# Performance work log

Hardware: AMD Instinct MI355X
Metric: run time of the kernel (lower is better)

Reference implementation:

```python
import jax, jax.numpy as jnp
import numpy as np

S = 32  # spatial_size
EPS = 1e-8

def _adaptive_avg_pool(x, s):
    b, c, h, w = x.shape
    kh, kw = h // s, w // s
    return x.reshape(b, c, s, kh, s, kw).mean(axis=(3, 5))

def _gram_cosine(x):
    # x: [B, C, s, s] -> rows: [B*s*s, C]
    b, c, s, _ = x.shape
    rows = x.reshape(b, c, s * s).transpose(0, 2, 1).reshape(b * s * s, c)
    norms = jnp.sqrt(jnp.sum(rows * rows, axis=-1, keepdims=True))
    xn = rows / jnp.maximum(norms, EPS)
    return xn @ xn.T  # [N, N]

def setup_inputs() -> dict:
    key = jax.random.key(0)
    k1, k2 = jax.random.split(key)
    p1 = jax.random.normal(k1, (8, 64, 128, 128), dtype=jnp.float32)
    p2 = jax.random.normal(k2, (8, 64, 128, 128), dtype=jnp.float32)
    return {"p1": p1, "p2": p2}

def reference(p1, p2):
    sim_a = _gram_cosine(_adaptive_avg_pool(p1, S))
    sim_b = _gram_cosine(_adaptive_avg_pool(p2, S))
    return jnp.mean((sim_a - sim_b) ** 2)
```

## Files before the change

kernel.cpp:

```cpp
#include <hip/hip_runtime.h>

typedef float f4 __attribute__((ext_vector_type(4)));
typedef float f2 __attribute__((ext_vector_type(2)));

#define PAD 68
#define NPART 256
#define PART_STRIDE 12288


__global__ __launch_bounds__(1024) void fused_gram_kernel(
    const float* __restrict__ p1, const float* __restrict__ p2,
    float* __restrict__ partials, unsigned* __restrict__ cnt)
{
    __shared__ float la[32 * PAD];
    __shared__ float lb[32 * PAD];
    __shared__ float nred[64][17];
    __shared__ float sa[32], sb[32];
    const int t  = threadIdx.x;
    const int b  = blockIdx.x >> 5;
    const int oi = blockIdx.x & 31;

    if (blockIdx.x == 0 && t == 0) *cnt = 0u;

    #pragma unroll
    for (int k = 0; k < 2; ++k) {
        const int idx = k * 1024 + t;
        const int c   = idx >> 5;
        const int oj  = idx & 31;
        const long off = (long)((b * 64 + c) * 128 + oi * 4) * 128 + oj * 4;
        const float* s1 = p1 + off;
        const float* s2 = p2 + off;
        f4 va = *(const f4*)(s1) + *(const f4*)(s1 + 128)
              + *(const f4*)(s1 + 256) + *(const f4*)(s1 + 384);
        f4 vb = *(const f4*)(s2) + *(const f4*)(s2 + 128)
              + *(const f4*)(s2 + 256) + *(const f4*)(s2 + 384);
        la[oj * PAD + c] = ((va[0] + va[1]) + (va[2] + va[3])) * 0.0625f;
        lb[oj * PAD + c] = ((vb[0] + vb[1]) + (vb[2] + vb[3])) * 0.0625f;
    }
    __syncthreads();

    {
        const int r = t & 31, g = t >> 5;
        const int m = g >> 4, q = g & 15;
        const float* src = m ? lb : la;
        float ss = 0.f;
        #pragma unroll
        for (int j = 0; j < 4; ++j) {
            const float v = src[r * PAD + q * 4 + j];
            ss = fmaf(v, v, ss);
        }
        nred[m * 32 + r][q] = ss;
    }
    __syncthreads();
    if (t < 64) {
        const int m = t >> 5, r = t & 31;
        float ss = 0.f;
        #pragma unroll
        for (int q = 0; q < 16; ++q) ss += nred[m * 32 + r][q];
        const float rs = 1.0f / fmaxf(sqrtf(ss), 1e-8f);
        if (m) sb[r] = rs; else sa[r] = rs;
    }
    __syncthreads();

    #pragma unroll
    for (int k = 0; k < 2; ++k) {
        const int idx = k * 1024 + t;
        const int c = idx >> 5, oj = idx & 31;
        la[oj * PAD + c] *= sa[oj];
        lb[oj * PAD + c] *= sb[oj];
    }
    __syncthreads();

    const int c1 = (t >> 5) * 2;
    const int c2 = (t & 31) * 2;
    f2 aa0 = {}, aa1 = {}, ab0 = {}, ab1 = {}, bb0 = {}, bb1 = {};

    #pragma unroll 8
    for (int r = 0; r < 32; ++r) {
        const f2 a1 = *(const f2*)&la[r * PAD + c1];
        const f2 a2 = *(const f2*)&la[r * PAD + c2];
        const f2 b1 = *(const f2*)&lb[r * PAD + c1];
        const f2 b2 = *(const f2*)&lb[r * PAD + c2];
        aa0 += a2 * a1[0];  aa1 += a2 * a1[1];
        ab0 += b2 * a1[0];  ab1 += b2 * a1[1];
        bb0 += b2 * b1[0];  bb1 += b2 * b1[1];
    }

    float* P = partials + (long)blockIdx.x * PART_STRIDE;
    *(f2*)&P[0 * 4096 + (c1    ) * 64 + c2] = aa0;
    *(f2*)&P[0 * 4096 + (c1 + 1) * 64 + c2] = aa1;
    *(f2*)&P[1 * 4096 + (c1    ) * 64 + c2] = ab0;
    *(f2*)&P[1 * 4096 + (c1 + 1) * 64 + c2] = ab1;
    *(f2*)&P[2 * 4096 + (c1    ) * 64 + c2] = bb0;
    *(f2*)&P[2 * 4096 + (c1 + 1) * 64 + c2] = bb1;
}

__global__ __launch_bounds__(256) void reduce_kernel(
    const float* __restrict__ partials, float* __restrict__ bpart,
    unsigned* __restrict__ cnt, float* __restrict__ out)
{
    __shared__ float red[3][16][17];
    __shared__ float vred[16];
    __shared__ float fr[256];
    __shared__ unsigned last_flag;
    const int t  = threadIdx.x;
    const int el = t & 15;
    const int pc = t >> 4;
    const int e  = blockIdx.x * 16 + el;

    float saa = 0.f, sab = 0.f, sbb = 0.f;
    #pragma unroll 4
    for (int i = 0; i < 16; ++i) {
        const float* P = partials + (long)(pc * 16 + i) * PART_STRIDE;
        saa += P[e];
        sab += P[4096 + e];
        sbb += P[8192 + e];
    }
    red[0][el][pc] = saa; red[1][el][pc] = sab; red[2][el][pc] = sbb;
    __syncthreads();

    if (t < 16) {
        float a = 0.f, m = 0.f, bv = 0.f;
        #pragma unroll
        for (int p = 0; p < 16; ++p) {
            a  += red[0][t][p];
            m  += red[1][t][p];
            bv += red[2][t][p];
        }
        vred[t] = fmaf(a, a, fmaf(bv, bv, -2.0f * (m * m)));
    }
    __syncthreads();

    if (t == 0) {
        float s = 0.f;
        #pragma unroll
        for (int i = 0; i < 16; ++i) s += vred[i];
        __hip_atomic_store(&bpart[blockIdx.x], s, __ATOMIC_RELEASE,
                           __HIP_MEMORY_SCOPE_AGENT);
        unsigned old = __hip_atomic_fetch_add(cnt, 1u, __ATOMIC_ACQ_REL,
                                              __HIP_MEMORY_SCOPE_AGENT);
        last_flag = (old == NPART - 1) ? 1u : 0u;
    }
    __syncthreads();

    if (last_flag) {
        fr[t] = __hip_atomic_load(&bpart[t], __ATOMIC_ACQUIRE,
                                  __HIP_MEMORY_SCOPE_AGENT);
        __syncthreads();
        for (int s2 = 128; s2 > 0; s2 >>= 1) {
            if (t < s2) fr[t] += fr[t + s2];
            __syncthreads();
        }
        if (t == 0) out[0] = fr[0] * (1.0f / 67108864.0f);
    }
}

extern "C" void kernel_launch(void* const* d_in, const int* in_sizes, int n_in,
                              void* d_out, int out_size, void* d_ws, size_t ws_size,
                              hipStream_t stream)
{
    const float* p1 = (const float*)d_in[0];
    const float* p2 = (const float*)d_in[1];
    float* ws       = (float*)d_ws;
    float* partials = ws;
    float* bpart    = ws + (long)NPART * PART_STRIDE;
    unsigned* cnt   = (unsigned*)(bpart + NPART);

    fused_gram_kernel<<<NPART, 1024, 0, stream>>>(p1, p2, partials, cnt);
    reduce_kernel   <<<NPART, 256, 0, stream>>>(partials, bpart, cnt, (float*)d_out);
}
```

Before: 35.19 us.

## Fuse gram and reduction kernels with a grid-wide spin barrier and transposed partials

Merges the two kernels into one, using an atomic counter spin barrier so that all 256 blocks finish writing partials before the cross-block reduction starts. Partials are stored transposed (element-major, block-minor) so that each wavefront can read 256 contiguous values and reduce them with shuffles. The counter is reset with a memset node instead of inside the kernel. This removes one kernel launch and the shared-memory staging of the reduction. In exchange the scattered stride-256 stores become uncoalesced, and the spin barrier relies on all 256 blocks of 1024 threads being co-resident.

```diff
diff --git a/kernel.cpp b/kernel.cpp
--- a/kernel.cpp
+++ b/kernel.cpp
@@ -4,23 +4,25 @@
 typedef float f2 __attribute__((ext_vector_type(2)));
 
 #define PAD 68
-#define NPART 256
-#define PART_STRIDE 12288
+#define NBLK 256
 
 
-__global__ __launch_bounds__(1024) void fused_gram_kernel(
+__global__ __launch_bounds__(1024) void fused_all_kernel(
     const float* __restrict__ p1, const float* __restrict__ p2,
-    float* __restrict__ partials, unsigned* __restrict__ cnt)
+    float* __restrict__ pT, float* __restrict__ bpart,
+    unsigned* __restrict__ cnt, float* __restrict__ out)
 {
     __shared__ float la[32 * PAD];
     __shared__ float lb[32 * PAD];
     __shared__ float nred[64][17];
     __shared__ float sa[32], sb[32];
-    const int t  = threadIdx.x;
-    const int b  = blockIdx.x >> 5;
-    const int oi = blockIdx.x & 31;
-
-    if (blockIdx.x == 0 && t == 0) *cnt = 0u;
+    __shared__ float vred[16];
+    __shared__ float fr[256];
+    __shared__ unsigned lastf;
+    const int t   = threadIdx.x;
+    const int blk = blockIdx.x;
+    const int b   = blk >> 5;
+    const int oi  = blk & 31;
 
     #pragma unroll
     for (int k = 0; k < 2; ++k) {
@@ -86,48 +88,52 @@
         bb0 += b2 * b1[0];  bb1 += b2 * b1[1];
     }
 
-    float* P = partials + (long)blockIdx.x * PART_STRIDE;
-    *(f2*)&P[0 * 4096 + (c1    ) * 64 + c2] = aa0;
-    *(f2*)&P[0 * 4096 + (c1 + 1) * 64 + c2] = aa1;
-    *(f2*)&P[1 * 4096 + (c1    ) * 64 + c2] = ab0;
-    *(f2*)&P[1 * 4096 + (c1 + 1) * 64 + c2] = ab1;
-    *(f2*)&P[2 * 4096 + (c1    ) * 64 + c2] = bb0;
-    *(f2*)&P[2 * 4096 + (c1 + 1) * 64 + c2] = bb1;
-}
+    {
+        const int e0 = c1 * 64 + c2;
+        const int e1 = e0 + 64;
+        pT[(0 * 4096 + e0    ) * 256 + blk] = aa0[0];
+        pT[(0 * 4096 + e0 + 1) * 256 + blk] = aa0[1];
+        pT[(0 * 4096 + e1    ) * 256 + blk] = aa1[0];
+        pT[(0 * 4096 + e1 + 1) * 256 + blk] = aa1[1];
+        pT[(1 * 4096 + e0    ) * 256 + blk] = ab0[0];
+        pT[(1 * 4096 + e0 + 1) * 256 + blk] = ab0[1];
+        pT[(1 * 4096 + e1    ) * 256 + blk] = ab1[0];
+        pT[(1 * 4096 + e1 + 1) * 256 + blk] = ab1[1];
+        pT[(2 * 4096 + e0    ) * 256 + blk] = bb0[0];
+        pT[(2 * 4096 + e0 + 1) * 256 + blk] = bb0[1];
+        pT[(2 * 4096 + e1    ) * 256 + blk] = bb1[0];
+        pT[(2 * 4096 + e1 + 1) * 256 + blk] = bb1[1];
+    }
 
-__global__ __launch_bounds__(256) void reduce_kernel(
-    const float* __restrict__ partials, float* __restrict__ bpart,
-    unsigned* __restrict__ cnt, float* __restrict__ out)
-{
-    __shared__ float red[3][16][17];
-    __shared__ float vred[16];
-    __shared__ float fr[256];
-    __shared__ unsigned last_flag;
-    const int t  = threadIdx.x;
-    const int el = t & 15;
-    const int pc = t >> 4;
-    const int e  = blockIdx.x * 16 + el;
-
-    float saa = 0.f, sab = 0.f, sbb = 0.f;
-    #pragma unroll 4
-    for (int i = 0; i < 16; ++i) {
-        const float* P = partials + (long)(pc * 16 + i) * PART_STRIDE;
-        saa += P[e];
-        sab += P[4096 + e];
-        sbb += P[8192 + e];
+    __syncthreads();
+    if (t == 0) {
+        __hip_atomic_fetch_add(cnt, 1u, __ATOMIC_ACQ_REL,
+                               __HIP_MEMORY_SCOPE_AGENT);
+        while (__hip_atomic_load(cnt, __ATOMIC_ACQUIRE,
+                                 __HIP_MEMORY_SCOPE_AGENT) < NBLK) {}
     }
-    red[0][el][pc] = saa; red[1][el][pc] = sab; red[2][el][pc] = sbb;
     __syncthreads();
 
-    if (t < 16) {
-        float a = 0.f, m = 0.f, bv = 0.f;
+    {
+        const int w = t >> 6;
+        const int l = t & 63;
+        const int e = blk * 16 + w;
+        float s3[3];
         #pragma unroll
-        for (int p = 0; p < 16; ++p) {
-            a  += red[0][t][p];
-            m  += red[1][t][p];
-            bv += red[2][t][p];
+        for (int g = 0; g < 3; ++g) {
+            const f4 v = *(const f4*)&pT[((g * 4096 + e) * 256) + l * 4];
+            float s = (v[0] + v[1]) + (v[2] + v[3]);
+            s += __shfl_xor(s, 1);
+            s += __shfl_xor(s, 2);
+            s += __shfl_xor(s, 4);
+            s += __shfl_xor(s, 8);
+            s += __shfl_xor(s, 16);
+            s += __shfl_xor(s, 32);
+            s3[g] = s;
         }
-        vred[t] = fmaf(a, a, fmaf(bv, bv, -2.0f * (m * m)));
+        if (l == 0)
+            vred[w] = fmaf(s3[0], s3[0],
+                      fmaf(s3[2], s3[2], -2.0f * (s3[1] * s3[1])));
     }
     __syncthreads();
 
@@ -135,17 +141,18 @@
         float s = 0.f;
         #pragma unroll
         for (int i = 0; i < 16; ++i) s += vred[i];
-        __hip_atomic_store(&bpart[blockIdx.x], s, __ATOMIC_RELEASE,
+        __hip_atomic_store(&bpart[blk], s, __ATOMIC_RELEASE,
                            __HIP_MEMORY_SCOPE_AGENT);
-        unsigned old = __hip_atomic_fetch_add(cnt, 1u, __ATOMIC_ACQ_REL,
+        unsigned old = __hip_atomic_fetch_add(cnt + 1, 1u, __ATOMIC_ACQ_REL,
                                               __HIP_MEMORY_SCOPE_AGENT);
-        last_flag = (old == NPART - 1) ? 1u : 0u;
+        lastf = (old == NBLK - 1) ? 1u : 0u;
     }
     __syncthreads();
 
-    if (last_flag) {
-        fr[t] = __hip_atomic_load(&bpart[t], __ATOMIC_ACQUIRE,
-                                  __HIP_MEMORY_SCOPE_AGENT);
+    if (lastf) {
+        if (t < 256)
+            fr[t] = __hip_atomic_load(&bpart[t], __ATOMIC_ACQUIRE,
+                                      __HIP_MEMORY_SCOPE_AGENT);
         __syncthreads();
         for (int s2 = 128; s2 > 0; s2 >>= 1) {
             if (t < s2) fr[t] += fr[t + s2];
@@ -161,11 +168,12 @@
 {
     const float* p1 = (const float*)d_in[0];
     const float* p2 = (const float*)d_in[1];
-    float* ws       = (float*)d_ws;
-    float* partials = ws;
-    float* bpart    = ws + (long)NPART * PART_STRIDE;
-    unsigned* cnt   = (unsigned*)(bpart + NPART);
+    float* ws    = (float*)d_ws;
+    float* pT    = ws;
+    float* bpart = ws + 3 * 4096 * 256;
+    unsigned* cnt = (unsigned*)(bpart + 256);
 
-    fused_gram_kernel<<<NPART, 1024, 0, stream>>>(p1, p2, partials, cnt);
-    reduce_kernel   <<<NPART, 256, 0, stream>>>(partials, bpart, cnt, (float*)d_out);
+    hipMemsetAsync(cnt, 0, 2 * sizeof(unsigned), stream);
+    fused_all_kernel<<<NBLK, 1024, 0, stream>>>(p1, p2, pT, bpart, cnt,
+                                                (float*)d_out);
 }
```

New measurement: 107.1 us. 3.04x slower.

## Split each pooled row across two blocks to double grid parallelism

Applied to the files above, without the earlier changes.

The gram kernel now launches 512 blocks of 512 threads, each handling half of a pooled row (16 spatial positions) instead of a full row, with f4-wide register tiles in the 64x64 channel-gram accumulation. This fills more CUs on the MI355X and uses wider LDS loads and global stores. In exchange the partial-sum buffer doubles, so the reduction kernel reads twice as many partials (32 per thread) and there is more global write and read traffic.

```diff
diff --git a/kernel.cpp b/kernel.cpp
--- a/kernel.cpp
+++ b/kernel.cpp
@@ -4,43 +4,46 @@
 typedef float f2 __attribute__((ext_vector_type(2)));
 
 #define PAD 68
-#define NPART 256
+#define NPART 512
 #define PART_STRIDE 12288
+#define NBLK2 256
 
 
-__global__ __launch_bounds__(1024) void fused_gram_kernel(
+__global__ __launch_bounds__(512) void fused_gram_kernel(
     const float* __restrict__ p1, const float* __restrict__ p2,
     float* __restrict__ partials, unsigned* __restrict__ cnt)
 {
-    __shared__ float la[32 * PAD];
-    __shared__ float lb[32 * PAD];
-    __shared__ float nred[64][17];
-    __shared__ float sa[32], sb[32];
-    const int t  = threadIdx.x;
-    const int b  = blockIdx.x >> 5;
-    const int oi = blockIdx.x & 31;
+    __shared__ float la[16 * PAD];
+    __shared__ float lb[16 * PAD];
+    __shared__ float nred[32][17];
+    __shared__ float sa[16], sb[16];
+    const int t   = threadIdx.x;
+    const int blk = blockIdx.x;
+    const int b   = blk >> 6;
+    const int oi  = (blk & 63) >> 1;
+    const int h   = blk & 1;
 
-    if (blockIdx.x == 0 && t == 0) *cnt = 0u;
+    if (blk == 0 && t == 0) *cnt = 0u;
 
     #pragma unroll
-    for (int k = 0; k < 2; ++k) {
-        const int idx = k * 1024 + t;
-        const int c   = idx >> 5;
-        const int oj  = idx & 31;
-        const long off = (long)((b * 64 + c) * 128 + oi * 4) * 128 + oj * 4;
-        const float* s1 = p1 + off;
-        const float* s2 = p2 + off;
-        f4 va = *(const f4*)(s1) + *(const f4*)(s1 + 128)
-              + *(const f4*)(s1 + 256) + *(const f4*)(s1 + 384);
-        f4 vb = *(const f4*)(s2) + *(const f4*)(s2 + 128)
-              + *(const f4*)(s2 + 256) + *(const f4*)(s2 + 384);
-        la[oj * PAD + c] = ((va[0] + va[1]) + (va[2] + va[3])) * 0.0625f;
-        lb[oj * PAD + c] = ((vb[0] + vb[1]) + (vb[2] + vb[3])) * 0.0625f;
+    for (int k = 0; k < 4; ++k) {
+        const int idx  = k * 512 + t;
+        const int m    = idx >> 10;
+        const int rest = idx & 1023;
+        const int c    = rest >> 4;
+        const int oj16 = rest & 15;
+        const long off = (long)((b * 64 + c) * 128 + oi * 4) * 128
+                       + (h * 16 + oj16) * 4;
+        const float* s = (m ? p2 : p1) + off;
+        f4 v = *(const f4*)(s) + *(const f4*)(s + 128)
+             + *(const f4*)(s + 256) + *(const f4*)(s + 384);
+        float* dst = m ? lb : la;
+        dst[oj16 * PAD + c] = ((v[0] + v[1]) + (v[2] + v[3])) * 0.0625f;
     }
     __syncthreads();
 
     {
-        const int r = t & 31, g = t >> 5;
+        const int r = t & 15, g = t >> 4;
         const int m = g >> 4, q = g & 15;
         const float* src = m ? lb : la;
         float ss = 0.f;
@@ -49,50 +52,53 @@
             const float v = src[r * PAD + q * 4 + j];
             ss = fmaf(v, v, ss);
         }
-        nred[m * 32 + r][q] = ss;
+        nred[m * 16 + r][q] = ss;
     }
     __syncthreads();
-    if (t < 64) {
-        const int m = t >> 5, r = t & 31;
+    if (t < 32) {
+        const int m = t >> 4, r = t & 15;
         float ss = 0.f;
         #pragma unroll
-        for (int q = 0; q < 16; ++q) ss += nred[m * 32 + r][q];
+        for (int q = 0; q < 16; ++q) ss += nred[m * 16 + r][q];
         const float rs = 1.0f / fmaxf(sqrtf(ss), 1e-8f);
         if (m) sb[r] = rs; else sa[r] = rs;
     }
     __syncthreads();
 
     #pragma unroll
-    for (int k = 0; k < 2; ++k) {
-        const int idx = k * 1024 + t;
-        const int c = idx >> 5, oj = idx & 31;
-        la[oj * PAD + c] *= sa[oj];
-        lb[oj * PAD + c] *= sb[oj];
+    for (int k = 0; k < 4; ++k) {
+        const int idx  = k * 512 + t;
+        const int m    = idx >> 10;
+        const int rest = idx & 1023;
+        const int r    = rest >> 6;
+        const int c    = rest & 63;
+        if (m) lb[r * PAD + c] *= sb[r];
+        else   la[r * PAD + c] *= sa[r];
     }
     __syncthreads();
 
-    const int c1 = (t >> 5) * 2;
-    const int c2 = (t & 31) * 2;
-    f2 aa0 = {}, aa1 = {}, ab0 = {}, ab1 = {}, bb0 = {}, bb1 = {};
+    const int c1 = (t >> 4) * 2;
+    const int c2 = (t & 15) * 4;
+    f4 aa0 = {}, aa1 = {}, ab0 = {}, ab1 = {}, bb0 = {}, bb1 = {};
 
     #pragma unroll 8
-    for (int r = 0; r < 32; ++r) {
+    for (int r = 0; r < 16; ++r) {
         const f2 a1 = *(const f2*)&la[r * PAD + c1];
-        const f2 a2 = *(const f2*)&la[r * PAD + c2];
+        const f4 a2 = *(const f4*)&la[r * PAD + c2];
         const f2 b1 = *(const f2*)&lb[r * PAD + c1];
-        const f2 b2 = *(const f2*)&lb[r * PAD + c2];
+        const f4 b2 = *(const f4*)&lb[r * PAD + c2];
         aa0 += a2 * a1[0];  aa1 += a2 * a1[1];
         ab0 += b2 * a1[0];  ab1 += b2 * a1[1];
         bb0 += b2 * b1[0];  bb1 += b2 * b1[1];
     }
 
-    float* P = partials + (long)blockIdx.x * PART_STRIDE;
-    *(f2*)&P[0 * 4096 + (c1    ) * 64 + c2] = aa0;
-    *(f2*)&P[0 * 4096 + (c1 + 1) * 64 + c2] = aa1;
-    *(f2*)&P[1 * 4096 + (c1    ) * 64 + c2] = ab0;
-    *(f2*)&P[1 * 4096 + (c1 + 1) * 64 + c2] = ab1;
-    *(f2*)&P[2 * 4096 + (c1    ) * 64 + c2] = bb0;
-    *(f2*)&P[2 * 4096 + (c1 + 1) * 64 + c2] = bb1;
+    float* P = partials + (long)blk * PART_STRIDE;
+    *(f4*)&P[0 * 4096 + (c1    ) * 64 + c2] = aa0;
+    *(f4*)&P[0 * 4096 + (c1 + 1) * 64 + c2] = aa1;
+    *(f4*)&P[1 * 4096 + (c1    ) * 64 + c2] = ab0;
+    *(f4*)&P[1 * 4096 + (c1 + 1) * 64 + c2] = ab1;
+    *(f4*)&P[2 * 4096 + (c1    ) * 64 + c2] = bb0;
+    *(f4*)&P[2 * 4096 + (c1 + 1) * 64 + c2] = bb1;
 }
 
 __global__ __launch_bounds__(256) void reduce_kernel(
@@ -110,8 +116,8 @@
 
     float saa = 0.f, sab = 0.f, sbb = 0.f;
     #pragma unroll 4
-    for (int i = 0; i < 16; ++i) {
-        const float* P = partials + (long)(pc * 16 + i) * PART_STRIDE;
+    for (int i = 0; i < 32; ++i) {
+        const float* P = partials + (long)(pc * 32 + i) * PART_STRIDE;
         saa += P[e];
         sab += P[4096 + e];
         sbb += P[8192 + e];
@@ -139,7 +145,7 @@
                            __HIP_MEMORY_SCOPE_AGENT);
         unsigned old = __hip_atomic_fetch_add(cnt, 1u, __ATOMIC_ACQ_REL,
                                               __HIP_MEMORY_SCOPE_AGENT);
-        last_flag = (old == NPART - 1) ? 1u : 0u;
+        last_flag = (old == NBLK2 - 1) ? 1u : 0u;
     }
     __syncthreads();
 
@@ -164,8 +170,8 @@
     float* ws       = (float*)d_ws;
     float* partials = ws;
     float* bpart    = ws + (long)NPART * PART_STRIDE;
-    unsigned* cnt   = (unsigned*)(bpart + NPART);
+    unsigned* cnt   = (unsigned*)(bpart + NBLK2);
 
-    fused_gram_kernel<<<NPART, 1024, 0, stream>>>(p1, p2, partials, cnt);
-    reduce_kernel   <<<NPART, 256, 0, stream>>>(partials, bpart, cnt, (float*)d_out);
+    fused_gram_kernel<<<NPART, 512, 0, stream>>>(p1, p2, partials, cnt);
+    reduce_kernel   <<<NBLK2, 256, 0, stream>>>(partials, bpart, cnt, (float*)d_out);
 }
```

Measured after the change: 37.64 us. 7.0% more time.

## Pipeline pooling loads with gram accumulation in four column chunks using double-buffered LDS

Applied to the files above, without the earlier changes.

Splits each block's 32 pooled columns into four chunks of 8 and double-buffers them in shared memory, issuing global loads for the next chunk before running the gram accumulation on the current one. Row normalization now uses a wave-wide shuffle reduction instead of a two-stage shared-memory reduction, and barriers use a raw waitcnt+s_barrier helper. The intent is to hide HBM load latency behind FMA work and cut synchronization overhead, at the cost of more barriers and register pressure for in-flight loads.

```diff
diff --git a/kernel.cpp b/kernel.cpp
--- a/kernel.cpp
+++ b/kernel.cpp
@@ -8,83 +8,98 @@
 #define PART_STRIDE 12288
 
 
+__device__ __forceinline__ void lds_barrier() {
+    asm volatile("s_waitcnt lgkmcnt(0)" ::: "memory");
+    __builtin_amdgcn_s_barrier();
+    __builtin_amdgcn_sched_barrier(0);
+}
+
 __global__ __launch_bounds__(1024) void fused_gram_kernel(
     const float* __restrict__ p1, const float* __restrict__ p2,
     float* __restrict__ partials, unsigned* __restrict__ cnt)
 {
-    __shared__ float la[32 * PAD];
-    __shared__ float lb[32 * PAD];
-    __shared__ float nred[64][17];
-    __shared__ float sa[32], sb[32];
+    __shared__ float la[2][8 * PAD];
+    __shared__ float lb[2][8 * PAD];
     const int t  = threadIdx.x;
     const int b  = blockIdx.x >> 5;
     const int oi = blockIdx.x & 31;
 
     if (blockIdx.x == 0 && t == 0) *cnt = 0u;
 
-    #pragma unroll
-    for (int k = 0; k < 2; ++k) {
-        const int idx = k * 1024 + t;
-        const int c   = idx >> 5;
-        const int oj  = idx & 31;
-        const long off = (long)((b * 64 + c) * 128 + oi * 4) * 128 + oj * 4;
-        const float* s1 = p1 + off;
-        const float* s2 = p2 + off;
-        f4 va = *(const f4*)(s1) + *(const f4*)(s1 + 128)
-              + *(const f4*)(s1 + 256) + *(const f4*)(s1 + 384);
-        f4 vb = *(const f4*)(s2) + *(const f4*)(s2 + 128)
-              + *(const f4*)(s2 + 256) + *(const f4*)(s2 + 384);
-        la[oj * PAD + c] = ((va[0] + va[1]) + (va[2] + va[3])) * 0.0625f;
-        lb[oj * PAD + c] = ((vb[0] + vb[1]) + (vb[2] + vb[3])) * 0.0625f;
-    }
-    __syncthreads();
+    const int m   = t >> 9;
+    const int c   = (t >> 3) & 63;
+    const int oj8 = t & 7;
+    const float* src = m ? p2 : p1;
+    const long base = (long)((b * 64 + c) * 128 + oi * 4) * 128 + oj8 * 4;
+    float* dst0 = m ? lb[0] : la[0];
+    float* dst1 = m ? lb[1] : la[1];
 
-    {
-        const int r = t & 31, g = t >> 5;
-        const int m = g >> 4, q = g & 15;
-        const float* src = m ? lb : la;
-        float ss = 0.f;
-        #pragma unroll
-        for (int j = 0; j < 4; ++j) {
-            const float v = src[r * PAD + q * 4 + j];
-            ss = fmaf(v, v, ss);
-        }
-        nred[m * 32 + r][q] = ss;
-    }
-    __syncthreads();
-    if (t < 64) {
-        const int m = t >> 5, r = t & 31;
-        float ss = 0.f;
-        #pragma unroll
-        for (int q = 0; q < 16; ++q) ss += nred[m * 32 + r][q];
-        const float rs = 1.0f / fmaxf(sqrtf(ss), 1e-8f);
-        if (m) sb[r] = rs; else sa[r] = rs;
-    }
-    __syncthreads();
-
-    #pragma unroll
-    for (int k = 0; k < 2; ++k) {
-        const int idx = k * 1024 + t;
-        const int c = idx >> 5, oj = idx & 31;
-        la[oj * PAD + c] *= sa[oj];
-        lb[oj * PAD + c] *= sb[oj];
-    }
-    __syncthreads();
+    const int l  = t & 63;
+    const int w  = t >> 6;
+    const int nm = w >> 3, nr = w & 7;
 
     const int c1 = (t >> 5) * 2;
     const int c2 = (t & 31) * 2;
     f2 aa0 = {}, aa1 = {}, ab0 = {}, ab1 = {}, bb0 = {}, bb1 = {};
 
-    #pragma unroll 8
-    for (int r = 0; r < 32; ++r) {
-        const f2 a1 = *(const f2*)&la[r * PAD + c1];
-        const f2 a2 = *(const f2*)&la[r * PAD + c2];
-        const f2 b1 = *(const f2*)&lb[r * PAD + c1];
-        const f2 b2 = *(const f2*)&lb[r * PAD + c2];
-        aa0 += a2 * a1[0];  aa1 += a2 * a1[1];
-        ab0 += b2 * a1[0];  ab1 += b2 * a1[1];
-        bb0 += b2 * b1[0];  bb1 += b2 * b1[1];
-    }
+    auto issue = [&](int q, f4& R0, f4& R1, f4& R2, f4& R3) {
+        const float* s = src + base + q * 32;
+        R0 = *(const f4*)(s);
+        R1 = *(const f4*)(s + 128);
+        R2 = *(const f4*)(s + 256);
+        R3 = *(const f4*)(s + 384);
+    };
+    auto pool = [&](const f4& R0, const f4& R1, const f4& R2, const f4& R3,
+                    float* dst) {
+        const f4 v = (R0 + R1) + (R2 + R3);
+        dst[oj8 * PAD + c] = ((v[0] + v[1]) + (v[2] + v[3])) * 0.0625f;
+    };
+    auto normphase = [&](int bi) {
+        float* rowp = (nm ? lb[bi] : la[bi]) + nr * PAD;
+        const float v = rowp[l];
+        float ss = v * v;
+        ss += __shfl_xor(ss, 1);
+        ss += __shfl_xor(ss, 2);
+        ss += __shfl_xor(ss, 4);
+        ss += __shfl_xor(ss, 8);
+        ss += __shfl_xor(ss, 16);
+        ss += __shfl_xor(ss, 32);
+        rowp[l] = v * (1.0f / fmaxf(sqrtf(ss), 1e-8f));
+    };
+    auto gram = [&](int bi) {
+        #pragma unroll
+        for (int r = 0; r < 8; ++r) {
+            const f2 a1 = *(const f2*)&la[bi][r * PAD + c1];
+            const f2 a2 = *(const f2*)&la[bi][r * PAD + c2];
+            const f2 b1 = *(const f2*)&lb[bi][r * PAD + c1];
+            const f2 b2 = *(const f2*)&lb[bi][r * PAD + c2];
+            aa0 += a2 * a1[0];  aa1 += a2 * a1[1];
+            ab0 += b2 * a1[0];  ab1 += b2 * a1[1];
+            bb0 += b2 * b1[0];  bb1 += b2 * b1[1];
+        }
+    };
+
+    f4 A0, A1, A2, A3, B0, B1, B2, B3;
+    issue(0, A0, A1, A2, A3);
+    issue(1, B0, B1, B2, B3);
+
+    pool(A0, A1, A2, A3, dst0);  lds_barrier();
+    normphase(0);                lds_barrier();
+    issue(2, A0, A1, A2, A3);
+    gram(0);
+
+    pool(B0, B1, B2, B3, dst1);  lds_barrier();
+    normphase(1);                lds_barrier();
+    issue(3, B0, B1, B2, B3);
+    gram(1);
+
+    pool(A0, A1, A2, A3, dst0);  lds_barrier();
+    normphase(0);                lds_barrier();
+    gram(0);
+
+    pool(B0, B1, B2, B3, dst1);  lds_barrier();
+    normphase(1);                lds_barrier();
+    gram(1);
 
     float* P = partials + (long)blockIdx.x * PART_STRIDE;
     *(f2*)&P[0 * 4096 + (c1    ) * 64 + c2] = aa0;
@@ -120,14 +135,14 @@
     __syncthreads();
 
     if (t < 16) {
-        float a = 0.f, m = 0.f, bv = 0.f;
+        float a = 0.f, mm = 0.f, bv = 0.f;
         #pragma unroll
         for (int p = 0; p < 16; ++p) {
             a  += red[0][t][p];
-            m  += red[1][t][p];
+            mm += red[1][t][p];
             bv += red[2][t][p];
         }
-        vred[t] = fmaf(a, a, fmaf(bv, bv, -2.0f * (m * m)));
+        vred[t] = fmaf(a, a, fmaf(bv, bv, -2.0f * (mm * mm)));
     }
     __syncthreads();
 
@@ -164,7 +179,7 @@
     float* ws       = (float*)d_ws;
     float* partials = ws;
     float* bpart    = ws + (long)NPART * PART_STRIDE;
-    unsigned* cnt   = (unsigned*)(bpart + NPART);
+    unsigned* cnt   = (unsigned*)(ws + 3146240);
 
     fused_gram_kernel<<<NPART, 1024, 0, stream>>>(p1, p2, partials, cnt);
     reduce_kernel   <<<NPART, 256, 0, stream>>>(partials, bpart, cnt, (float*)d_out);
```

Result: faster. 33.67 us (-4.3%).
